# Performance work log

Measured on AMD Instinct MI355X. Metric: run time of the kernel, lower is better.

The kernel has to match this reference:

```python
import jax, jax.numpy as jnp
import numpy as np

K_TARGETS = 15  # hardcoded k in _select_targets
N_CLASSES = 8


def setup_inputs() -> dict:
    key = jax.random.key(0)
    k1, k2, k3 = jax.random.split(key, 3)
    n, p, d = 128, 512, 64
    return {
        "segment_center": jax.random.normal(k1, (n, d), dtype=jnp.float32),
        "outputs": jax.random.normal(k2, (n, p, d), dtype=jnp.float32),
        "label_inds": jax.random.randint(k3, (n, p), 0, N_CLASSES),
    }


def reference(segment_center, outputs, label_inds):
    # segment_center: [n, d]; outputs: [n, p, d]; label_inds: [n, p] int
    n, p, d = outputs.shape
    labels = label_inds.reshape(n, p)
    same = labels[:, :, None] == labels[:, None, :]          # [n, p, p] same-label mask

    # squared distance of each point to its segment center: cdist(...)^2
    dist_c = jnp.sum((outputs - segment_center[:, None, :]) ** 2, axis=-1)  # [n, p]

    # _select_targets: dd[n,i,j] = dist_c[n,i], masked to +inf where labels differ,
    # topk smallest over j -> k same-label target-neighbor indices per point.
    dd = jnp.where(same, dist_c[:, :, None], jnp.inf)        # [n, p, p]
    _, target_neighbors = jax.lax.top_k(-dd, K_TARGETS)      # [n, p, K] smallest

    # squared center-distance of each target neighbor (intended gather in forward)
    gathered = dist_c[jnp.arange(n)[:, None, None], target_neighbors]  # [n, p, K]

    furthest = gathered.max(axis=2)                          # [n, p]
    margin_radii = 1.0 + furthest                            # per-point margin
    pull_loss = gathered.sum()

    # _find_impostors: per-segment margin = 1 + max center-dist over all gathered
    # target neighbors; impostor (n,i,j) iff label_i != label_j and
    # dist_c[n,i] < margin_seg[n]. Hinge term depends only on (n,i), so sum the
    # hinge weighted by the count of different-label j (avoids nonzero/gather).
    margin_seg = 1.0 + gathered.max(axis=(1, 2))             # [n]
    diff_count = (p - same.sum(axis=2)).astype(outputs.dtype)  # [n, p] #{j: label_j != label_i}
    is_impostor = (dist_c < margin_seg[:, None]).astype(outputs.dtype)  # [n, p]
    hinge = jnp.maximum(margin_radii - dist_c, 0.0)          # [n, p]
    push_loss = jnp.sum(diff_count * is_impostor * hinge)

    return (pull_loss + push_loss) / (n * p)
```

## Files before the change

### kernel.cpp

```cpp
#include <hip/hip_runtime.h>
#include <math.h>

constexpr int NSEG = 128;
constexpr int P    = 512;
constexpr int D    = 64;
constexpr int KT   = 15;
constexpr int NCLS = 8;

__global__ __launch_bounds__(512, 1) void lmnn_kernel(
    const float* __restrict__ center,
    const float* __restrict__ outputs,
    const int*   __restrict__ labels,
    float* __restrict__ out)
{
    __shared__ float s_dist[P];
    __shared__ int   s_lab[P];
    __shared__ float s_S[NCLS];
    __shared__ float s_M[NCLS];
    __shared__ int   s_cnt[NCLS];
    __shared__ float s_hb[NCLS];
    __shared__ float s_dc[NCLS];
    __shared__ float s_margin;
    __shared__ float s_pull;
    __shared__ float s_wsum[8];

    const int seg  = blockIdx.x;
    const int tid  = threadIdx.x;
    const int lane = tid & 63;
    const int wave = tid >> 6;

    s_lab[tid] = labels[seg * P + tid];

    const float4* c4 = reinterpret_cast<const float4*>(center + seg * D);
    const float4  cf = c4[lane & 15];

    const float4* o4 = reinterpret_cast<const float4*>(outputs + (size_t)seg * P * D);
    for (int g = wave; g < P / 4; g += 8) {
        float4 v = o4[g * 64 + lane];
        float dx = v.x - cf.x;
        float dy = v.y - cf.y;
        float dz = v.z - cf.z;
        float dw = v.w - cf.w;
        float acc = dx * dx + dy * dy + dz * dz + dw * dw;
        acc += __shfl_xor(acc, 1);
        acc += __shfl_xor(acc, 2);
        acc += __shfl_xor(acc, 4);
        acc += __shfl_xor(acc, 8);
        if ((lane & 15) == 0) s_dist[g * 4 + (lane >> 4)] = acc;
    }
    __syncthreads();

    {
        const int c = wave;
        float S = 0.0f;
        float M = -INFINITY;
        int taken = 0;
        int total = 0;
        for (int j = 0; j < 8; ++j) {
            const int pos = j * 64 + lane;
            const bool pred = (s_lab[pos] == c);
            const unsigned long long mask = __ballot(pred);
            const int cnt  = __popcll(mask);
            const int rank = __popcll(mask & ((1ull << lane) - 1ull));
            const bool sel = pred && (taken + rank < KT);
            float vs = sel ? s_dist[pos] : 0.0f;
            float vm = sel ? s_dist[pos] : -INFINITY;
            #pragma unroll
            for (int m = 1; m < 64; m <<= 1) {
                vs += __shfl_xor(vs, m);
                vm = fmaxf(vm, __shfl_xor(vm, m));
            }
            S += vs;
            M = fmaxf(M, vm);
            total += cnt;
            taken += cnt;
            if (taken > KT) taken = KT;
        }
        if (total < KT) {
            const int need = KT - total;
            int t2 = 0;
            for (int j = 0; j < 8 && t2 < need; ++j) {
                const int pos = j * 64 + lane;
                const bool pred = (s_lab[pos] != c);
                const unsigned long long mask = __ballot(pred);
                const int cnt  = __popcll(mask);
                const int rank = __popcll(mask & ((1ull << lane) - 1ull));
                const bool sel = pred && (t2 + rank < need);
                float vs = sel ? s_dist[pos] : 0.0f;
                float vm = sel ? s_dist[pos] : -INFINITY;
                #pragma unroll
                for (int m = 1; m < 64; m <<= 1) {
                    vs += __shfl_xor(vs, m);
                    vm = fmaxf(vm, __shfl_xor(vm, m));
                }
                S += vs;
                M = fmaxf(M, vm);
                t2 += cnt;
                if (t2 > need) t2 = need;
            }
        }
        if (lane == 0) {
            s_S[c]   = S;
            s_M[c]   = M;
            s_cnt[c] = total;
        }
    }
    __syncthreads();

    if (tid == 0) {
        float margin = -INFINITY;
        float pull = 0.0f;
        for (int c = 0; c < NCLS; ++c) {
            if (s_cnt[c] > 0) margin = fmaxf(margin, s_M[c]);
            pull += (float)s_cnt[c] * s_S[c];
            s_hb[c] = 1.0f + s_M[c];
            s_dc[c] = (float)(P - s_cnt[c]);
        }
        s_margin = 1.0f + margin;
        s_pull = pull;
    }
    __syncthreads();

    {
        const float dv = s_dist[tid];
        const int   c  = s_lab[tid];
        const float h  = fmaxf(s_hb[c] - dv, 0.0f);
        float v = (dv < s_margin) ? s_dc[c] * h : 0.0f;
        #pragma unroll
        for (int m = 1; m < 64; m <<= 1) v += __shfl_xor(v, m);
        if (lane == 0) s_wsum[wave] = v;
    }
    __syncthreads();

    if (tid == 0) {
        float t = s_pull;
        #pragma unroll
        for (int w = 0; w < 8; ++w) t += s_wsum[w];
        atomicAdd(out, t * (1.0f / ((float)NSEG * (float)P)));
    }
}

extern "C" void kernel_launch(void* const* d_in, const int* in_sizes, int n_in,
                              void* d_out, int out_size, void* d_ws, size_t ws_size,
                              hipStream_t stream) {
    const float* center  = (const float*)d_in[0];
    const float* outputs = (const float*)d_in[1];
    const int*   labels  = (const int*)d_in[2];
    float* out = (float*)d_out;

    hipMemsetAsync(out, 0, sizeof(float), stream);
    lmnn_kernel<<<dim3(NSEG), dim3(512), 0, stream>>>(center, outputs, labels, out);
}
```

Before: 77.05 us.

## Split distance computation into a separate wider-grid kernel before combine

Moves the per-point center-distance computation into its own kernel launched with four blocks per segment (512 blocks of 256 threads), writing distances to workspace. A second kernel reads those distances and the labels to do the per-class selection and loss reduction. The goal is to spread the 16 MB outputs read across more of the GPU's compute units than the original 128 blocks could use. In exchange it adds a kernel launch and a round trip of the distance array through global memory.

Result: no change. 76.69 us (-0.5%).

```diff
diff --git a/kernel.cpp b/kernel.cpp
--- a/kernel.cpp
+++ b/kernel.cpp
@@ -7,9 +7,42 @@
 constexpr int KT   = 15;
 constexpr int NCLS = 8;
 
-__global__ __launch_bounds__(512, 1) void lmnn_kernel(
+__global__ __launch_bounds__(256) void dist_kernel(
     const float* __restrict__ center,
     const float* __restrict__ outputs,
+    float* __restrict__ dist)
+{
+    const int seg     = blockIdx.x >> 2;
+    const int quarter = blockIdx.x & 3;
+    const int t   = threadIdx.x;
+    const int sub = t & 15;
+    const int pg  = t >> 4;
+
+    const float4* c4 = reinterpret_cast<const float4*>(center);
+    const float4  cf = c4[seg * 16 + sub];
+
+    const float4* o4 = reinterpret_cast<const float4*>(outputs);
+    const int pt_base = quarter * 128;
+
+    #pragma unroll
+    for (int it = 0; it < 8; ++it) {
+        const int pt = pt_base + it * 16 + pg;
+        float4 v = o4[((size_t)seg * P + pt) * 16 + sub];
+        float dx = v.x - cf.x;
+        float dy = v.y - cf.y;
+        float dz = v.z - cf.z;
+        float dw = v.w - cf.w;
+        float acc = dx * dx + dy * dy + dz * dz + dw * dw;
+        acc += __shfl_xor(acc, 1);
+        acc += __shfl_xor(acc, 2);
+        acc += __shfl_xor(acc, 4);
+        acc += __shfl_xor(acc, 8);
+        if (sub == 0) dist[seg * P + pt] = acc;
+    }
+}
+
+__global__ __launch_bounds__(512, 1) void combine_kernel(
+    const float* __restrict__ dist,
     const int*   __restrict__ labels,
     float* __restrict__ out)
 {
@@ -29,25 +62,8 @@
     const int lane = tid & 63;
     const int wave = tid >> 6;
 
-    s_lab[tid] = labels[seg * P + tid];
-
-    const float4* c4 = reinterpret_cast<const float4*>(center + seg * D);
-    const float4  cf = c4[lane & 15];
-
-    const float4* o4 = reinterpret_cast<const float4*>(outputs + (size_t)seg * P * D);
-    for (int g = wave; g < P / 4; g += 8) {
-        float4 v = o4[g * 64 + lane];
-        float dx = v.x - cf.x;
-        float dy = v.y - cf.y;
-        float dz = v.z - cf.z;
-        float dw = v.w - cf.w;
-        float acc = dx * dx + dy * dy + dz * dz + dw * dw;
-        acc += __shfl_xor(acc, 1);
-        acc += __shfl_xor(acc, 2);
-        acc += __shfl_xor(acc, 4);
-        acc += __shfl_xor(acc, 8);
-        if ((lane & 15) == 0) s_dist[g * 4 + (lane >> 4)] = acc;
-    }
+    s_lab[tid]  = labels[seg * P + tid];
+    s_dist[tid] = dist[seg * P + tid];
     __syncthreads();
 
     {
@@ -146,8 +162,10 @@
     const float* center  = (const float*)d_in[0];
     const float* outputs = (const float*)d_in[1];
     const int*   labels  = (const int*)d_in[2];
-    float* out = (float*)d_out;
+    float* out  = (float*)d_out;
+    float* dist = (float*)d_ws;
 
     hipMemsetAsync(out, 0, sizeof(float), stream);
-    lmnn_kernel<<<dim3(NSEG), dim3(512), 0, stream>>>(center, outputs, labels, out);
+    dist_kernel<<<dim3(NSEG * 4), dim3(256), 0, stream>>>(center, outputs, dist);
+    combine_kernel<<<dim3(NSEG), dim3(512), 0, stream>>>(dist, labels, out);
 }
```
